# Optimization experiments

Hardware: AMD Instinct MI355X
Metric: run time of the kernel (lower is better)

Reference implementation:

```python
import jax, jax.numpy as jnp
import numpy as np

V, H, W, L, HID = 8, 256, 256, 32, 64
NC, NF = 64, 64
R = 1024


def _grid_sample(img, grid):
    # img [V,C,H,W], grid [V,N,2] with (x,y) in [-1,1]; bilinear, zero padding,
    # align_corners=False (matches torch.nn.functional.grid_sample defaults).
    Vv, C, Hh, Ww = img.shape
    x = (grid[..., 0] + 1.0) * (Ww * 0.5) - 0.5
    y = (grid[..., 1] + 1.0) * (Hh * 0.5) - 0.5
    x0 = jnp.floor(x)
    y0 = jnp.floor(y)
    wx = x - x0
    wy = y - y0
    vidx = jnp.arange(Vv)[:, None]
    def tap(xf, yf):
        valid = (xf >= 0) & (xf <= Ww - 1) & (yf >= 0) & (yf <= Hh - 1)
        xi = jnp.clip(xf, 0, Ww - 1).astype(jnp.int32)
        yi = jnp.clip(yf, 0, Hh - 1).astype(jnp.int32)
        return img[vidx, :, yi, xi] * valid[..., None].astype(img.dtype)  # [V,N,C]
    return (tap(x0, y0) * ((1 - wx) * (1 - wy))[..., None]
            + tap(x0 + 1, y0) * (wx * (1 - wy))[..., None]
            + tap(x0, y0 + 1) * ((1 - wx) * wy)[..., None]
            + tap(x0 + 1, y0 + 1) * (wx * wy)[..., None])  # [V,N,C]


def _sample_pdf(bins, weights, n):
    # NeRF inverse-CDF importance sampling; deterministic midpoint u's.
    w = weights + 1e-5                              # [R, M]
    pdf = w / w.sum(-1, keepdims=True)
    cdf = jnp.concatenate([jnp.zeros_like(pdf[:, :1]), jnp.cumsum(pdf, -1)], -1)  # [R, M+1]
    u = jnp.broadcast_to((jnp.arange(n) + 0.5) / n, (bins.shape[0], n))
    inds = jax.vmap(lambda c, uu: jnp.searchsorted(c, uu, side='right'))(cdf, u)
    below = jnp.clip(inds - 1, 0, cdf.shape[-1] - 1)
    above = jnp.clip(inds, 0, cdf.shape[-1] - 1)
    cdf0 = jnp.take_along_axis(cdf, below, -1)
    cdf1 = jnp.take_along_axis(cdf, above, -1)
    bin0 = jnp.take_along_axis(bins, below, -1)
    bin1 = jnp.take_along_axis(bins, above, -1)
    denom = jnp.where(cdf1 - cdf0 < 1e-5, 1.0, cdf1 - cdf0)
    t = (u - cdf0) / denom
    return bin0 + t * (bin1 - bin0)


def _ibrnet(raw_rgb, feat, src_dirc, ray_dirc, W1, b1, W2, b2, Wd, bd, Wb, bb):
    # IBRNet-style per-view MLP + cross-view pooling for density, softmax
    # blending of source colors for rgb.
    x = jnp.concatenate([raw_rgb, feat, src_dirc,
                         jnp.broadcast_to(ray_dirc[:, None, :], src_dirc.shape)], -1)  # [P,V,3+L+3+3]
    h = jax.nn.relu(x @ W1 + b1)
    h = jax.nn.relu(h @ W2 + b2)                    # [P,V,HID]
    pooled = jnp.concatenate([h.mean(1), h.var(1)], -1)  # [P,2*HID]
    density = pooled @ Wd + bd                      # [P,1]
    blend = jax.nn.softmax((h @ Wb + bb)[..., 0], axis=1)  # [P,V]
    rgb = jnp.einsum('pv,pvc->pc', blend, raw_rgb)  # [P,3]
    return density, rgb


def _composite(depth, density, rgb):
    # NeRF alpha compositing along samples.
    delta = jnp.concatenate([depth[:, 1:] - depth[:, :-1],
                             jnp.full_like(depth[:, :1], 1e10)], -1)
    alpha = 1.0 - jnp.exp(-jax.nn.relu(density) * delta)
    trans = jnp.cumprod(1.0 - alpha + 1e-10, -1)
    trans = jnp.concatenate([jnp.ones_like(trans[:, :1]), trans[:, :-1]], -1)
    w = alpha * trans                               # [R,S]
    return w, (w[..., None] * rgb).sum(1), (w * depth).sum(1), w.sum(1)


def setup_inputs():
    rng = np.random.default_rng(0)

    def look_at(pos):
        pos = np.asarray(pos, np.float64)
        z = -pos / np.linalg.norm(pos)
        up = np.array([0.0, 0.0, 1.0])
        x = np.cross(up, z); x /= np.linalg.norm(x)
        y = np.cross(z, x)
        Rm = np.stack([x, y, z], 0)
        return np.concatenate([Rm, (-Rm @ pos)[:, None]], 1).astype(np.float32)

    ang = np.linspace(0, 2 * np.pi, V, endpoint=False)
    cam_pos = np.stack([3 * np.cos(ang), 3 * np.sin(ang), 0.3 * np.ones(V)], 1)
    E = np.stack([look_at(p) for p in cam_pos], 0)              # [V,3,4]
    f = 300.0
    K = np.broadcast_to(np.array([[f, 0, W / 2], [0, f, H / 2], [0, 0, 1]], np.float32), (V, 3, 3)).copy()

    o = np.array([3.2, 0.1, 0.2], np.float32)
    targets = rng.uniform(-0.2, 0.2, (R, 3)).astype(np.float32)  # points near head center
    d = targets - o
    d /= np.linalg.norm(d, axis=1, keepdims=True)
    dist = float(np.linalg.norm(o))
    near = np.full((R, 1), dist - 0.5, np.float32)
    far = np.full((R, 1), dist + 0.5, np.float32)
    ray = np.concatenate([np.broadcast_to(o, (R, 3)), d, near, far], 1).astype(np.float32)

    inp = {
        'ray': jnp.asarray(ray),
        'source_intrinsic': jnp.asarray(K),
        'source_extrinsic': jnp.asarray(E),
        'source_cam_pos': jnp.asarray(cam_pos.astype(np.float32)),
        'source_shape': jnp.full((V, 2), float(H), jnp.float32),
        'source_mask': jnp.ones((V, 1, H, W), jnp.float32),
        'source_image': jnp.asarray(rng.random((V, 3, H, W), dtype=np.float32)),
        'source_feature': jnp.asarray(rng.standard_normal((V, 2 * L, H, W), dtype=np.float32) * 0.1),
    }
    in_dim = 3 + L + 3 + 3

    def mlp(prefix):
        return {
            prefix + 'W1': jnp.asarray(rng.standard_normal((in_dim, HID), dtype=np.float32) * 0.1),
            prefix + 'b1': jnp.asarray(rng.standard_normal(HID, dtype=np.float32) * 0.01),
            prefix + 'W2': jnp.asarray(rng.standard_normal((HID, HID), dtype=np.float32) * 0.1),
            prefix + 'b2': jnp.asarray(rng.standard_normal(HID, dtype=np.float32) * 0.01),
            prefix + 'Wd': jnp.asarray(rng.standard_normal((2 * HID, 1), dtype=np.float32) * 0.1),
            prefix + 'bd': jnp.asarray(rng.standard_normal(1, dtype=np.float32) * 0.01),
            prefix + 'Wb': jnp.asarray(rng.standard_normal((HID, 1), dtype=np.float32) * 0.1),
            prefix + 'bb': jnp.asarray(rng.standard_normal(1, dtype=np.float32) * 0.01),
        }
    inp.update(mlp('c'))
    inp.update(mlp('f'))
    return inp


def reference(ray, source_intrinsic, source_extrinsic, source_cam_pos, source_shape,
              source_mask, source_image, source_feature,
              cW1, cb1, cW2, cb2, cWd, cbd, cWb, cbb,
              fW1, fb1, fW2, fb2, fWd, fbd, fWb, fbb):
    o, d = ray[:, :3], ray[:, 3:6]
    near, far = ray[:, 6:7], ray[:, 7:8]
    P = jnp.einsum('vij,vjk->vik', source_intrinsic, source_extrinsic)  # [V,3,4]
    wh = source_shape[:, ::-1]                                          # (W,H) per view

    def sample_point(depth):                    # depth [R,S]
        pos = o[:, None, :] + d[:, None, :] * depth[..., None]          # [R,S,3]
        dn = d / jnp.linalg.norm(d, axis=-1, keepdims=True)
        dirc = jnp.broadcast_to(dn[:, None, :], pos.shape)
        pos_h = jnp.concatenate([pos, jnp.ones_like(pos[..., :1])], -1)
        pix = jnp.einsum('rsk,vck->rsvc', pos_h, P)                     # [R,S,V,3]
        pix = pix[..., :2] / (pix[..., 2:3] + 1e-6)
        pix = 2.0 * (pix / wh[None, None]) - 1.0
        return pos, -dirc, pix

    def compute_color(pos, dirc, pix, W1, b1, W2, b2, Wd, bd, Wb, bb, fs, fe):
        Rr, Ss = pix.shape[0], pix.shape[1]
        grid = pix.reshape(Rr * Ss, -1, 2).transpose(1, 0, 2)           # [V,P,2]
        m = _grid_sample(source_mask, grid)[..., 0]                     # [V,P]
        hull = m.sum(0) > (source_mask.shape[0] - 1e-3)                 # visual hull: inside all views
        raw_rgb = _grid_sample(source_image, grid).transpose(1, 0, 2)   # [P,V,3]
        feat = _grid_sample(source_feature, grid)[..., fs:fe].transpose(1, 0, 2)  # [P,V,L]
        pos_f = pos.reshape(-1, 3)
        sd = source_cam_pos[None] - pos_f[:, None]
        sd = sd / jnp.linalg.norm(sd, axis=-1, keepdims=True)
        dens, rgb = _ibrnet(raw_rgb, feat, sd, dirc.reshape(-1, 3), W1, b1, W2, b2, Wd, bd, Wb, bb)
        dens = jnp.where(hull, dens[:, 0], 0.0).reshape(Rr, Ss)
        rgb = jnp.where(hull[:, None], rgb, 0.0).reshape(Rr, Ss, 3)
        return dens, rgb

    # coarse stratified sampling (deterministic bin midpoints)
    t = (jnp.arange(NC) + 0.5) / NC
    c_depth = near + (far - near) * t[None]                             # [R,NC]
    c_pos, c_dir, c_pix = sample_point(c_depth)
    c_dens, c_rgbp = compute_color(c_pos, c_dir, c_pix, cW1, cb1, cW2, cb2, cWd, cbd, cWb, cbb, 0, L)
    c_w, c_rgb, c_dep, c_alp = _composite(c_depth, c_dens, c_rgbp)

    # fine importance sampling from coarse weights
    mids = 0.5 * (c_depth[:, 1:] + c_depth[:, :-1])
    f_depth = _sample_pdf(mids, jax.lax.stop_gradient(c_w[:, 1:-1]), NF)
    full_depth = jnp.sort(jnp.concatenate([c_depth, f_depth], -1), -1)  # [R,NC+NF]
    f_pos, f_dir, f_pix = sample_point(full_depth)
    f_dens, f_rgbp = compute_color(f_pos, f_dir, f_pix, fW1, fb1, fW2, fb2, fWd, fbd, fWb, fbb, L, 2 * L)
    _, f_rgb, f_dep, f_alp = _composite(full_depth, f_dens, f_rgbp)
    return c_rgb, c_dep, c_alp, f_rgb, f_dep, f_alp
```

## Files before the change

### kernel.cpp

```cpp
#include <hip/hip_runtime.h>
#include <hip/hip_bf16.h>
#include <math.h>

#define V_   8
#define H_   256
#define W_   256
#define L_   32
#define HID_ 64
#define NC_  64
#define NF_  64
#define R_   1024
#define IND_ 41
#define HW_  (H_*W_)

typedef __attribute__((ext_vector_type(8)))  short short8v;
typedef __attribute__((ext_vector_type(16))) float f32x16;

__device__ __forceinline__ unsigned int pk2bf(float a, float b) {
    unsigned int ra = (unsigned int)__bfloat16_as_ushort(__float2bfloat16(a));
    unsigned int rb = (unsigned int)__bfloat16_as_ushort(__float2bfloat16(b));
    return ra | (rb << 16);
}

template<int CTRL>
__device__ __forceinline__ float dpp_add(float x) {
    int m = __builtin_amdgcn_mov_dpp(__builtin_bit_cast(int, x), CTRL, 0xF, 0xF, true);
    return x + __builtin_bit_cast(float, m);
}
template<int CTRL>
__device__ __forceinline__ float dpp_max(float x) {
    int m = __builtin_amdgcn_mov_dpp(__builtin_bit_cast(int, x), CTRL, 0xF, 0xF, true);
    return fmaxf(x, __builtin_bit_cast(float, m));
}
__device__ __forceinline__ float swz_xor4(float x) {
    int m = __builtin_amdgcn_ds_swizzle(__builtin_bit_cast(int, x), 0x101F);
    return __builtin_bit_cast(float, m);
}
__device__ __forceinline__ float vsum8(float x) {
    x = dpp_add<0xB1>(x);
    x = dpp_add<0x4E>(x);
    x += swz_xor4(x);
    return x;
}
__device__ __forceinline__ float vmax8(float x) {
    x = dpp_max<0xB1>(x);
    x = dpp_max<0x4E>(x);
    x = fmaxf(x, swz_xor4(x));
    return x;
}
__device__ __forceinline__ float redsum64(float x) {
    #pragma unroll
    for (int off = 32; off >= 1; off >>= 1) x += __shfl_xor(x, off, 64);
    return x;
}
__device__ __forceinline__ float scan_mul64(float x, int lane) {
    #pragma unroll
    for (int off = 1; off < 64; off <<= 1) {
        float y = __shfl_up(x, off, 64);
        x = (lane >= off) ? x * y : x;
    }
    return x;
}
__device__ __forceinline__ float scan_add64(float x, int lane) {
    #pragma unroll
    for (int off = 1; off < 64; off <<= 1) {
        float y = __shfl_up(x, off, 64);
        x = (lane >= off) ? x + y : x;
    }
    return x;
}

__device__ __forceinline__ void packMFMA_body(
    int t, const float* __restrict__ W1, const float* __restrict__ b1,
    const float* __restrict__ W2, const float* __restrict__ b2,
    const float* __restrict__ Wd, const float* __restrict__ Wb,
    unsigned int* __restrict__ out) {
    if (t < 1536) {
        int blk = t >> 8, idx = t & 255;
        int mt = blk / 3, kt = blk % 3;
        int l = idx >> 2, rg = idx & 3;
        int hi = l >> 5;
        int j  = 32 * mt + (l & 31);
        int k0 = 16 * kt + 8 * hi + 2 * rg;
        int k1 = k0 + 1;
        float v0 = (k0 < 41) ? W1[k0 * 64 + j] : (k0 == 41 ? b1[j] : 0.f);
        float v1 = (k1 < 41) ? W1[k1 * 64 + j] : (k1 == 41 ? b1[j] : 0.f);
        out[t] = pk2bf(v0, v1);
    } else if (t < 3584) {
        int u = t - 1536;
        int blk = u >> 8, idx = u & 255;
        int l = idx >> 2, rg = idx & 3;
        int hi = l >> 5;
        int j2 = 32 * (blk >> 2) + (l & 31);
        int k0 = 16 * (blk & 3) + 8 * hi + 2 * rg;
        out[t] = pk2bf(W2[k0 * 64 + j2], W2[(k0 + 1) * 64 + j2]);
    } else if (t < 3840) {
        int i = t - 3584;
        int w = i >> 6, mt = (i >> 5) & 1, hi = (i >> 4) & 1, rg = i & 15;
        int j2 = (rg & 3) + 8 * (rg >> 2) + 4 * hi + 32 * mt;
        float v = (w == 0) ? b2[j2] : (w == 1) ? Wb[j2] : (w == 2) ? Wd[j2] : Wd[64 + j2];
        ((float*)out)[t] = v;
    }
}

__global__ __launch_bounds__(256) void k_init(
    const float* __restrict__ Km, const float* __restrict__ Em, float* __restrict__ Pm,
    const float* __restrict__ cW1, const float* __restrict__ cb1,
    const float* __restrict__ cW2, const float* __restrict__ cb2,
    const float* __restrict__ cWd, const float* __restrict__ cWb,
    unsigned int* __restrict__ FRc,
    const float* __restrict__ fW1, const float* __restrict__ fb1,
    const float* __restrict__ fW2, const float* __restrict__ fb2,
    const float* __restrict__ fWd, const float* __restrict__ fWb,
    unsigned int* __restrict__ FRf) {
    const int bid = blockIdx.x, tid = threadIdx.x;
    if (bid == 0) {
        if (tid >= V_ * 12) return;
        int v = tid / 12, e = tid - v * 12, row = e >> 2, col = e & 3;
        float acc = 0.f;
        #pragma unroll
        for (int k = 0; k < 3; ++k)
            acc += Km[v * 9 + row * 3 + k] * Em[v * 12 + k * 4 + col];
        Pm[v * 12 + row * 4 + col] = acc;
    } else if (bid <= 15) {
        packMFMA_body((bid - 1) * 256 + tid, cW1, cb1, cW2, cb2, cWd, cWb, FRc);
    } else if (bid <= 30) {
        packMFMA_body((bid - 16) * 256 + tid, fW1, fb1, fW2, fb2, fWd, fWb, FRf);
    }
}

__global__ __launch_bounds__(256) void k_packB2(const float* __restrict__ msk,
                                                const float* __restrict__ img,
                                                const float* __restrict__ fea,
                                                float* __restrict__ pk) {
    __shared__ unsigned short tile[64][80];
    const int xb = blockIdx.x * 64, y = blockIdx.y, v = blockIdx.z;
    const int t = threadIdx.x;
    const int x = t & 63, cg = t >> 6;
    const size_t px = (size_t)y * W_ + xb + x;
    #pragma unroll
    for (int step = 0; step < 17; ++step) {
        int ch = step * 4 + cg;
        if (ch < 68) {
            float val;
            if (ch == 0)      val = msk[(size_t)v * HW_ + px];
            else if (ch < 4)  val = img[((size_t)(v * 3 + (ch - 1))) * HW_ + px];
            else              val = fea[((size_t)(v * 2 * L_ + (ch - 4))) * HW_ + px];
            unsigned short bf = __bfloat16_as_ushort(__float2bfloat16(val));
            if (ch == 0)      { tile[x][0] = bf; tile[x][40] = bf; }
            else if (ch < 4)  { tile[x][ch] = bf; tile[x][40 + ch] = bf; }
            else if (ch < 36) { tile[x][ch] = bf; }
            else              { tile[x][ch + 8] = bf; }
        }
    }
    if (t < 256) {
        int xi = t >> 2, c = t & 3;
        tile[xi][36 + c] = 0;
        tile[xi][76 + c] = 0;
    }
    __syncthreads();
    uint2* dst = (uint2*)(pk + ((size_t)v * HW_ + (size_t)y * W_ + xb) * 40);
    for (int j = t; j < 1280; j += 256) {
        int p = j / 20, sl = j % 20;
        dst[j] = *(const uint2*)&tile[p][sl * 4];
    }
}

template <int S, bool FINE, int GOFF>
__global__ __launch_bounds__(256) void k_mlp_mfma(
    const float* __restrict__ ray, const float* __restrict__ Pm,
    const float* __restrict__ cam, const float* __restrict__ shp,
    const float* __restrict__ pk,
    const unsigned int* __restrict__ FR,
    const float* __restrict__ bd, const float* __restrict__ bb,
    const float* __restrict__ deptharr,
    float* __restrict__ odens, float* __restrict__ orgb) {

    __shared__ __align__(16) char smem[40960];
    const int lane = threadIdx.x & 63;
    const int wv   = threadIdx.x >> 6;
    const int hi   = lane >> 5;
    const int l31  = lane & 31;
    char* Xw  = smem + wv * 10240;
    char* H1w = Xw + 6144;

    const int pbase = (blockIdx.x * 4 + wv) * 8;
    const int P0 = pbase + (lane >> 3);
    const int v  = lane & 7;
    const int r  = P0 / S, s = P0 - r * S;

    const float ox = ray[r*8+0], oy = ray[r*8+1], oz = ray[r*8+2];
    const float dx = ray[r*8+3], dy = ray[r*8+4], dz = ray[r*8+5];
    const float nv = ray[r*8+6], fv = ray[r*8+7];

    float depth;
    if (FINE) depth = deptharr[P0];
    else      depth = nv + (fv - nv) * ((s + 0.5f) / (float)S);

    const float px = ox + dx*depth, py = oy + dy*depth, pz = oz + dz*depth;
    const float dn = sqrtf(dx*dx + dy*dy + dz*dz);
    const float rdx = -dx/dn, rdy = -dy/dn, rdz = -dz/dn;

    const float* Pv = Pm + v * 12;
    float q0 = Pv[0]*px + Pv[1]*py + Pv[2]*pz  + Pv[3];
    float q1 = Pv[4]*px + Pv[5]*py + Pv[6]*pz  + Pv[7];
    float q2 = Pv[8]*px + Pv[9]*py + Pv[10]*pz + Pv[11];
    float inv = 1.0f / (q2 + 1e-6f);
    float uu = q0 * inv, ww = q1 * inv;
    float gx = 2.0f * (uu / shp[v*2+1]) - 1.0f;
    float gy = 2.0f * (ww / shp[v*2+0]) - 1.0f;
    float sx = (gx + 1.0f) * ((float)W_ * 0.5f) - 0.5f;
    float sy = (gy + 1.0f) * ((float)H_ * 0.5f) - 0.5f;
    float x0f = floorf(sx), y0f = floorf(sy);
    float fx = sx - x0f, fy = sy - y0f;

    int offp[4]; float wt[4];
    {
        float xs[2] = {x0f, x0f + 1.f}, ys[2] = {y0f, y0f + 1.f};
        float wxs[2] = {1.f - fx, fx},  wys[2] = {1.f - fy, fy};
        #pragma unroll
        for (int t = 0; t < 4; ++t) {
            float xf = xs[t & 1], yf = ys[t >> 1];
            bool val = (xf >= 0.f) && (xf <= (float)(W_-1)) &&
                       (yf >= 0.f) && (yf <= (float)(H_-1));
            int xi = (int)fminf(fmaxf(xf, 0.f), (float)(W_-1));
            int yi = (int)fminf(fmaxf(yf, 0.f), (float)(H_-1));
            offp[t] = yi * W_ + xi;
            wt[t] = wxs[t & 1] * wys[t >> 1] * (val ? 1.f : 0.f);
        }
    }

    float vals[40];
    #pragma unroll
    for (int i = 0; i < 40; ++i) vals[i] = 0.f;
    #pragma unroll
    for (int t = 0; t < 4; ++t) {
        const uint4* fp = (const uint4*)pk + ((size_t)v * HW_ + offp[t]) * 10 + GOFF;
        float wtt = wt[t];
        #pragma unroll
        for (int s5 = 0; s5 < 5; ++s5) {
            uint4 q = fp[s5];
            unsigned int dw[4] = {q.x, q.y, q.z, q.w};
            #pragma unroll
            for (int e = 0; e < 4; ++e) {
                int i = s5 * 8 + e * 2;
                vals[i]   += wtt * __uint_as_float(dw[e] << 16);
                vals[i+1] += wtt * __uint_as_float(dw[e] & 0xFFFF0000u);
            }
        }
    }
    float msample = vals[0];
    float rv0 = vals[1], rv1 = vals[2], rv2 = vals[3];
    float sdx = cam[v*3+0]-px, sdy = cam[v*3+1]-py, sdz = cam[v*3+2]-pz;
    float snv = sqrtf(sdx*sdx + sdy*sdy + sdz*sdz);
    sdx /= snv; sdy /= snv; sdz /= snv;

    float xx[42];
    xx[0] = rv0; xx[1] = rv1; xx[2] = rv2;
    #pragma unroll
    for (int k = 0; k < 32; ++k) xx[3+k] = vals[4+k];
    xx[35] = sdx; xx[36] = sdy; xx[37] = sdz;
    xx[38] = rdx; xx[39] = rdy; xx[40] = rdz;
    xx[41] = 1.0f;

    {
        unsigned int d[24];
        #pragma unroll
        for (int i = 0; i < 21; ++i) d[i] = pk2bf(xx[2*i], xx[2*i+1]);
        d[21] = 0u; d[22] = 0u; d[23] = 0u;
        #pragma unroll
        for (int o = 0; o < 6; ++o)
            *(uint4*)(Xw + o * 1024 + lane * 16) =
                make_uint4(d[o*4], d[o*4+1], d[o*4+2], d[o*4+3]);
    }

    short8v aw1[6];
    #pragma unroll
    for (int i = 0; i < 6; ++i)
        aw1[i] = __builtin_bit_cast(short8v, ((const uint4*)FR)[i * 64 + lane]);
    const float4* PL4 = (const float4*)(FR + 3584);
    const float bdv = bd[0], bbv = bb[0];

    float hs = vsum8(msample);
    float hssw  = __shfl_xor(hs, 32, 64);
    float rv0sw = __shfl_xor(rv0, 32, 64);
    float rv1sw = __shfl_xor(rv1, 32, 64);
    float rv2sw = __shfl_xor(rv2, 32, 64);

    #pragma unroll
    for (int nt = 0; nt < 2; ++nt) {
        const int n = nt * 32 + l31;
        f32x16 acc1[2];
        #pragma unroll
        for (int mt = 0; mt < 2; ++mt)
            #pragma unroll
            for (int q = 0; q < 16; ++q) acc1[mt][q] = 0.f;
        #pragma unroll
        for (int kt = 0; kt < 3; ++kt) {
            uint4 bu = *(const uint4*)(Xw + (2*kt + hi) * 1024 + n * 16);
            short8v b = __builtin_bit_cast(short8v, bu);
            acc1[0] = __builtin_amdgcn_mfma_f32_32x32x16_bf16(aw1[kt],     b, acc1[0], 0, 0, 0);
            acc1[1] = __builtin_amdgcn_mfma_f32_32x32x16_bf16(aw1[3 + kt], b, acc1[1], 0, 0, 0);
        }
        #pragma unroll
        for (int mt = 0; mt < 2; ++mt)
            #pragma unroll
            for (int q = 0; q < 4; ++q) {
                unsigned int w0 = pk2bf(fmaxf(acc1[mt][4*q+0], 0.f),
                                        fmaxf(acc1[mt][4*q+1], 0.f));
                unsigned int w1 = pk2bf(fmaxf(acc1[mt][4*q+2], 0.f),
                                        fmaxf(acc1[mt][4*q+3], 0.f));
                *(uint2*)(H1w + (q + 4*mt) * 512 + l31 * 16 + hi * 8) = make_uint2(w0, w1);
            }
        short8v aw2[8];
        #pragma unroll
        for (int i = 0; i < 8; ++i)
            aw2[i] = __builtin_bit_cast(short8v, ((const uint4*)(FR + 1536))[i * 64 + lane]);
        f32x16 acc2[2];
        #pragma unroll
        for (int mt = 0; mt < 2; ++mt)
            #pragma unroll
            for (int q4 = 0; q4 < 4; ++q4) {
                float4 c = PL4[(mt*2 + hi)*4 + q4];
                acc2[mt][4*q4+0] = c.x; acc2[mt][4*q4+1] = c.y;
                acc2[mt][4*q4+2] = c.z; acc2[mt][4*q4+3] = c.w;
            }
        #pragma unroll
        for (int kt = 0; kt < 4; ++kt) {
            uint4 bu = *(const uint4*)(H1w + (2*kt + hi) * 512 + l31 * 16);
            short8v b = __builtin_bit_cast(short8v, bu);
            acc2[0] = __builtin_amdgcn_mfma_f32_32x32x16_bf16(aw2[kt],     b, acc2[0], 0, 0, 0);
            acc2[1] = __builtin_amdgcn_mfma_f32_32x32x16_bf16(aw2[4 + kt], b, acc2[1], 0, 0, 0);
        }

        float lgp = 0.f, dacc = 0.f, cacc = 0.f;
        #pragma unroll
        for (int mt = 0; mt < 2; ++mt)
            #pragma unroll
            for (int q4 = 0; q4 < 4; ++q4) {
                float4 wb4 = PL4[16 + (mt*2 + hi)*4 + q4];
                float4 wd4 = PL4[32 + (mt*2 + hi)*4 + q4];
                float4 w24 = PL4[48 + (mt*2 + hi)*4 + q4];
                #pragma unroll
                for (int e = 0; e < 4; ++e) {
                    float hv = fmaxf(acc2[mt][4*q4+e], 0.f);
                    float wbv = (e==0)?wb4.x:(e==1)?wb4.y:(e==2)?wb4.z:wb4.w;
                    float wdv = (e==0)?wd4.x:(e==1)?wd4.y:(e==2)?wd4.z:wd4.w;
                    float w2v = (e==0)?w24.x:(e==1)?w24.y:(e==2)?w24.z:w24.w;
                    lgp  += hv * wbv;
                    dacc += hv * wdv + hv * hv * w2v;
                    float sj = vsum8(hv);
                    cacc += sj * sj * w2v;
                }
            }
        float lg = lgp + __shfl_xor(lgp, 32, 64) + bbv;
        dacc += __shfl_xor(dacc, 32, 64);
        dacc  = vsum8(dacc);
        cacc += __shfl_xor(cacc, 32, 64);
        float density = dacc * 0.125f - cacc * (1.0f / 64.0f) + bdv;

        float mx = vmax8(lg);
        float e  = expf(lg - mx);
        float es = vsum8(e);
        float r0c = (hi == nt) ? rv0 : rv0sw;
        float r1c = (hi == nt) ? rv1 : rv1sw;
        float r2c = (hi == nt) ? rv2 : rv2sw;
        float br  = vsum8(e * r0c);
        float bg  = vsum8(e * r1c);
        float bbl = vsum8(e * r2c);
        float hn  = (nt == 0) ? hs : hssw;
        bool hull = hn > ((float)V_ - 0.001f);

        if ((lane & 0x27) == 0) {
            int PP = pbase + 4 * nt + (lane >> 3);
            float is = 1.0f / es;
            odens[PP]      = hull ? density  : 0.f;
            orgb[PP*3 + 0] = hull ? br  * is : 0.f;
            orgb[PP*3 + 1] = hull ? bg  * is : 0.f;
            orgb[PP*3 + 2] = hull ? bbl * is : 0.f;
        }
    }
}

template <int S, int FS, bool FINE>
__global__ __launch_bounds__(256, 2) void k_mlp_fb(
    const float* __restrict__ ray, const float* __restrict__ Pm,
    const float* __restrict__ cam, const float* __restrict__ shp,
    const float* __restrict__ msk, const float* __restrict__ img,
    const float* __restrict__ fea,
    const float* __restrict__ W1, const float* __restrict__ b1,
    const float* __restrict__ W2, const float* __restrict__ b2,
    const float* __restrict__ Wd, const float* __restrict__ bd,
    const float* __restrict__ Wb, const float* __restrict__ bb,
    const float* __restrict__ deptharr,
    float* __restrict__ odens, float* __restrict__ orgb) {

    const int tid = blockIdx.x * 256 + threadIdx.x;
    const int v   = tid & 7;
    const int P   = tid >> 3;
    const int r   = P / S, s = P - r * S;

    const float ox = ray[r*8+0], oy = ray[r*8+1], oz = ray[r*8+2];
    const float dx = ray[r*8+3], dy = ray[r*8+4], dz = ray[r*8+5];
    const float nv = ray[r*8+6], fv = ray[r*8+7];
    float depth;
    if (FINE) depth = deptharr[P];
    else      depth = nv + (fv - nv) * ((s + 0.5f) / (float)S);
    const float px = ox + dx*depth, py = oy + dy*depth, pz = oz + dz*depth;
    const float dn = sqrtf(dx*dx + dy*dy + dz*dz);
    const float rdx = -dx/dn, rdy = -dy/dn, rdz = -dz/dn;
    const float* Pv = Pm + v * 12;
    float q0 = Pv[0]*px + Pv[1]*py + Pv[2]*pz  + Pv[3];
    float q1 = Pv[4]*px + Pv[5]*py + Pv[6]*pz  + Pv[7];
    float q2 = Pv[8]*px + Pv[9]*py + Pv[10]*pz + Pv[11];
    float inv = 1.0f / (q2 + 1e-6f);
    float uu = q0 * inv, ww = q1 * inv;
    float gx = 2.0f * (uu / shp[v*2+1]) - 1.0f;
    float gy = 2.0f * (ww / shp[v*2+0]) - 1.0f;
    float sx = (gx + 1.0f) * ((float)W_ * 0.5f) - 0.5f;
    float sy = (gy + 1.0f) * ((float)H_ * 0.5f) - 0.5f;
    float x0f = floorf(sx), y0f = floorf(sy);
    float fx = sx - x0f, fy = sy - y0f;
    int offp[4]; float wt[4];
    {
        float xs[2] = {x0f, x0f + 1.f}, ys[2] = {y0f, y0f + 1.f};
        float wxs[2] = {1.f - fx, fx},  wys[2] = {1.f - fy, fy};
        #pragma unroll
        for (int t = 0; t < 4; ++t) {
            float xf = xs[t & 1], yf = ys[t >> 1];
            bool val = (xf >= 0.f) && (xf <= (float)(W_-1)) &&
                       (yf >= 0.f) && (yf <= (float)(H_-1));
            int xi = (int)fminf(fmaxf(xf, 0.f), (float)(W_-1));
            int yi = (int)fminf(fmaxf(yf, 0.f), (float)(H_-1));
            offp[t] = yi * W_ + xi;
            wt[t] = wxs[t & 1] * wys[t >> 1] * (val ? 1.f : 0.f);
        }
    }
    const float* mb = msk + v * HW_;
    float msample = wt[0]*mb[offp[0]] + wt[1]*mb[offp[1]]
                  + wt[2]*mb[offp[2]] + wt[3]*mb[offp[3]];
    float rv0 = 0.f, rv1 = 0.f, rv2 = 0.f;
    {
        const float* ib = img + (v * 3) * HW_;
        #pragma unroll
        for (int t = 0; t < 4; ++t) {
            rv0 += wt[t] * ib[offp[t]];
            rv1 += wt[t] * ib[HW_ + offp[t]];
            rv2 += wt[t] * ib[2 * HW_ + offp[t]];
        }
    }
    float sdx = cam[v*3+0]-px, sdy = cam[v*3+1]-py, sdz = cam[v*3+2]-pz;
    float snv = sqrtf(sdx*sdx + sdy*sdy + sdz*sdz);
    sdx /= snv; sdy /= snv; sdz /= snv;
    float xx[IND_];
    xx[0] = rv0; xx[1] = rv1; xx[2] = rv2;
    #pragma unroll
    for (int k = 0; k < 32; ++k) {
        const float* fb = fea + (size_t)(v * (2*L_) + FS + k) * HW_;
        xx[3+k] = wt[0]*fb[offp[0]] + wt[1]*fb[offp[1]]
                + wt[2]*fb[offp[2]] + wt[3]*fb[offp[3]];
    }
    xx[35] = sdx; xx[36] = sdy; xx[37] = sdz;
    xx[38] = rdx; xx[39] = rdy; xx[40] = rdz;
    float h1[HID_];
    #pragma unroll
    for (int j = 0; j < HID_; ++j) {
        float a0 = 0.f;
        #pragma unroll
        for (int k = 0; k < IND_; ++k) a0 += xx[k] * W1[k * HID_ + j];
        h1[j] = fmaxf(b1[j] + a0, 0.f);
    }
    float lg = bb[0];
    float A = 0.f, B = 0.f, C = 0.f;
    #pragma unroll 1
    for (int j = 0; j < HID_; j += 4) {
        float hh[4];
        #pragma unroll
        for (int jj = 0; jj < 4; ++jj) {
            float a0 = 0.f;
            #pragma unroll
            for (int k = 0; k < HID_; ++k) a0 += h1[k] * W2[k * HID_ + (j + jj)];
            hh[jj] = fmaxf(b2[j + jj] + a0, 0.f);
        }
        #pragma unroll
        for (int jj = 0; jj < 4; ++jj) {
            float h = hh[jj];
            lg += h * Wb[j + jj];
            A  += h * Wd[j + jj];
            B  += h * h * Wd[HID_ + j + jj];
            float sj = vsum8(h);
            C  += sj * sj * Wd[HID_ + j + jj];
        }
    }
    A = vsum8(A); B = vsum8(B);
    float density = A * 0.125f + B * 0.125f - C * (1.0f / 64.0f) + bd[0];
    float hsv = vsum8(msample);
    bool hull = hsv > ((float)V_ - 0.001f);
    float mx = vmax8(lg);
    float e = expf(lg - mx);
    float es = vsum8(e);
    float br  = vsum8(e * rv0);
    float bg  = vsum8(e * rv1);
    float bbl = vsum8(e * rv2);
    if (v == 0) {
        float is = 1.0f / es;
        odens[P]      = hull ? density  : 0.f;
        orgb[P*3 + 0] = hull ? br  * is : 0.f;
        orgb[P*3 + 1] = hull ? bg  * is : 0.f;
        orgb[P*3 + 2] = hull ? bbl * is : 0.f;
    }
}

__global__ __launch_bounds__(256) void k_comp_coarse(const float* __restrict__ ray,
                                                     const float* __restrict__ dens,
                                                     const float* __restrict__ rgb,
                                                     float* __restrict__ out,
                                                     float* __restrict__ fulld) {
    __shared__ float cdfS[4][64];
    __shared__ float fdS[4][64];
    const int wv = threadIdx.x >> 6, lane = threadIdx.x & 63;
    const int r = blockIdx.x * 4 + wv;
    const float nv = ray[r*8+6], fv = ray[r*8+7];
    const int s = lane;

    float d0 = nv + (fv - nv) * ((s + 0.5f) / NC_);
    float d1 = nv + (fv - nv) * ((s + 1.5f) / NC_);
    float delta = (s == NC_-1) ? 1e10f : (d1 - d0);
    float a = 1.f - expf(-fmaxf(dens[r*NC_ + s], 0.f) * delta);
    float qv = 1.f - a + 1e-10f;
    float inc = scan_mul64(qv, lane);
    float trans = __shfl_up(inc, 1, 64);
    if (lane == 0) trans = 1.f;
    float w = a * trans;

    float g0 = rgb[(r*NC_+s)*3+0], g1 = rgb[(r*NC_+s)*3+1], g2 = rgb[(r*NC_+s)*3+2];
    float c0 = redsum64(w * g0);
    float c1 = redsum64(w * g1);
    float c2 = redsum64(w * g2);
    float cd = redsum64(w * d0);
    float ca = redsum64(w);
    if (lane == 0) {
        out[r*3+0] = c0; out[r*3+1] = c1; out[r*3+2] = c2;
        out[3072 + r] = cd;
        out[4096 + r] = ca;
    }

    float pw = (s >= 1 && s <= 62) ? (w + 1e-5f) : 0.f;
    float tot = redsum64(pw);
    float p = pw / tot;
    float ic = scan_add64(p, lane);
    cdfS[wv][lane] = ic;
    __syncthreads();

    float u = (lane + 0.5f) / NF_;
    int lo = 0, hi = 63;
    while (lo < hi) {
        int mid = (lo + hi) >> 1;
        if (cdfS[wv][mid] <= u) lo = mid + 1; else hi = mid;
    }
    int below = lo - 1;
    int above = (lo > 62) ? 62 : lo;
    float cA = cdfS[wv][below], cB = cdfS[wv][above];
    float b0 = nv + (fv - nv) * ((below + 1.0f) / NC_);
    float b1 = nv + (fv - nv) * ((above + 1.0f) / NC_);
    float dnm = cB - cA;
    dnm = (dnm < 1e-5f) ? 1.f : dnm;
    float fdv = b0 + (u - cA) / dnm * (b1 - b0);
    fdS[wv][lane] = fdv;
    __syncthreads();

    lo = 0; hi = 64;
    while (lo < hi) {
        int mid = (lo + hi) >> 1;
        if (fdS[wv][mid] < d0) lo = mid + 1; else hi = mid;
    }
    fulld[r*128 + s + lo] = d0;

    lo = 0; hi = 64;
    while (lo < hi) {
        int mid = (lo + hi) >> 1;
        float daj = nv + (fv - nv) * ((mid + 0.5f) / NC_);
        if (daj <= fdv) lo = mid + 1; else hi = mid;
    }
    fulld[r*128 + lane + lo] = fdv;
}

__global__ __launch_bounds__(256) void k_comp_fine(const float* __restrict__ fulld,
                                                   const float* __restrict__ dens,
                                                   const float* __restrict__ rgb,
                                                   float* __restrict__ out) {
    const int wv = threadIdx.x >> 6, lane = threadIdx.x & 63;
    const int r = blockIdx.x * 4 + wv;
    const int S = NC_ + NF_;
    const float* fl = fulld + r * S;
    const int s0 = 2 * lane, s1 = 2 * lane + 1;

    float f0 = fl[s0], f1 = fl[s1];
    float nx = __shfl_down(f0, 1, 64);
    float dl0 = f1 - f0;
    float dl1 = (lane == 63) ? 1e10f : (nx - f1);
    float a0 = 1.f - expf(-fmaxf(dens[r*S + s0], 0.f) * dl0);
    float a1 = 1.f - expf(-fmaxf(dens[r*S + s1], 0.f) * dl1);
    float q0 = 1.f - a0 + 1e-10f, q1 = 1.f - a1 + 1e-10f;
    float inc = scan_mul64(q0 * q1, lane);
    float E = __shfl_up(inc, 1, 64);
    if (lane == 0) E = 1.f;
    float w0 = a0 * E, w1 = a1 * (E * q0);

    float g00 = rgb[(r*S+s0)*3+0], g01 = rgb[(r*S+s0)*3+1], g02 = rgb[(r*S+s0)*3+2];
    float g10 = rgb[(r*S+s1)*3+0], g11 = rgb[(r*S+s1)*3+1], g12 = rgb[(r*S+s1)*3+2];
    float c0 = redsum64(w0*g00 + w1*g10);
    float c1 = redsum64(w0*g01 + w1*g11);
    float c2 = redsum64(w0*g02 + w1*g12);
    float cd = redsum64(w0*f0 + w1*f1);
    float ca = redsum64(w0 + w1);
    if (lane == 0) {
        out[5120 + r*3+0] = c0; out[5120 + r*3+1] = c1; out[5120 + r*3+2] = c2;
        out[8192 + r] = cd;
        out[9216 + r] = ca;
    }
}

extern "C" void kernel_launch(void* const* d_in, const int* in_sizes, int n_in,
                              void* d_out, int out_size, void* d_ws, size_t ws_size,
                              hipStream_t stream) {
    const float* ray = (const float*)d_in[0];
    const float* Kin = (const float*)d_in[1];
    const float* Ein = (const float*)d_in[2];
    const float* cam = (const float*)d_in[3];
    const float* shp = (const float*)d_in[4];
    const float* msk = (const float*)d_in[5];
    const float* img = (const float*)d_in[6];
    const float* fea = (const float*)d_in[7];
    const float* cw[8]; for (int i = 0; i < 8; ++i) cw[i] = (const float*)d_in[8+i];
    const float* fw[8]; for (int i = 0; i < 8; ++i) fw[i] = (const float*)d_in[16+i];

    float* ws    = (float*)d_ws;
    float* Pm    = ws;
    unsigned int* FRc = (unsigned int*)(Pm + 96);
    unsigned int* FRf = FRc + 4096;
    float* cdens = (float*)(FRf + 4096);
    float* crgb  = cdens + R_ * NC_;
    float* fulld = crgb + R_ * NC_ * 3;
    float* fdens = fulld + R_ * (NC_+NF_);
    float* frgb  = fdens + R_ * (NC_+NF_);
    float* pk    = frgb + R_ * (NC_+NF_) * 3;

    size_t base_floats = (size_t)(pk - ws);
    size_t need = (base_floats + (size_t)V_ * HW_ * 40 + 64) * sizeof(float);
    bool packed = (ws_size >= need);

    float* outp  = (float*)d_out;

    if (packed) {
        k_init<<<31, 256, 0, stream>>>(Kin, Ein, Pm,
            cw[0], cw[1], cw[2], cw[3], cw[4], cw[6], FRc,
            fw[0], fw[1], fw[2], fw[3], fw[4], fw[6], FRf);
        k_packB2<<<dim3(W_/64, H_, V_), 256, 0, stream>>>(msk, img, fea, pk);

        k_mlp_mfma<NC_, false, 0><<<R_ * NC_ / 32, 256, 0, stream>>>(
            ray, Pm, cam, shp, pk, FRc, cw[5], cw[7],
            nullptr, cdens, crgb);

        k_comp_coarse<<<R_ / 4, 256, 0, stream>>>(ray, cdens, crgb, outp, fulld);

        k_mlp_mfma<NC_ + NF_, true, 5><<<R_ * (NC_+NF_) / 32, 256, 0, stream>>>(
            ray, Pm, cam, shp, pk, FRf, fw[5], fw[7],
            fulld, fdens, frgb);

        k_comp_fine<<<R_ / 4, 256, 0, stream>>>(fulld, fdens, frgb, outp);
    } else {
        k_init<<<1, 256, 0, stream>>>(Kin, Ein, Pm,
            cw[0], cw[1], cw[2], cw[3], cw[4], cw[6], FRc,
            fw[0], fw[1], fw[2], fw[3], fw[4], fw[6], FRf);
        k_mlp_fb<NC_, 0, false><<<R_ * NC_ * 8 / 256, 256, 0, stream>>>(
            ray, Pm, cam, shp, msk, img, fea,
            cw[0], cw[1], cw[2], cw[3], cw[4], cw[5], cw[6], cw[7],
            nullptr, cdens, crgb);

        k_comp_coarse<<<R_ / 4, 256, 0, stream>>>(ray, cdens, crgb, outp, fulld);

        k_mlp_fb<NC_ + NF_, L_, true><<<R_ * (NC_+NF_) * 8 / 256, 256, 0, stream>>>(
            ray, Pm, cam, shp, msk, img, fea,
            fw[0], fw[1], fw[2], fw[3], fw[4], fw[5], fw[6], fw[7],
            fulld, fdens, frgb);

        k_comp_fine<<<R_ / 4, 256, 0, stream>>>(fulld, fdens, frgb, outp);
    }
}
```

Measured before the change: 193.0 us.

## Switch packed features and MLP MFMAs from bf16 to fp16 with packed bilinear accumulation

Converts the packed feature texture, the weight fragments and the hidden activations from bf16 to fp16, and switches the MFMA instructions to the f16 variant. Bilinear interpolation now accumulates directly in packed half2 vectors, so the results feed the MFMA input without unpack and repack steps. The W1 layout shifts by one row so the packed vector positions line up with the mask slot. This removes per-element conversion and float accumulation work in the gather loop, at the cost of accumulating in fp16, which can lose precision or overflow on large feature values.

Result: faster. 186.5 us (-3.3%).

```diff
diff --git a/kernel.cpp b/kernel.cpp
--- a/kernel.cpp
+++ b/kernel.cpp
@@ -13,13 +13,13 @@
 #define IND_ 41
 #define HW_  (H_*W_)
 
-typedef __attribute__((ext_vector_type(8)))  short short8v;
+typedef _Float16 h2v __attribute__((ext_vector_type(2)));
+typedef _Float16 h8v __attribute__((ext_vector_type(8)));
 typedef __attribute__((ext_vector_type(16))) float f32x16;
 
-__device__ __forceinline__ unsigned int pk2bf(float a, float b) {
-    unsigned int ra = (unsigned int)__bfloat16_as_ushort(__float2bfloat16(a));
-    unsigned int rb = (unsigned int)__bfloat16_as_ushort(__float2bfloat16(b));
-    return ra | (rb << 16);
+__device__ __forceinline__ unsigned int pk2hf(float a, float b) {
+    h2v t; t[0] = (_Float16)a; t[1] = (_Float16)b;
+    return __builtin_bit_cast(unsigned int, t);
 }
 
 template<int CTRL>
@@ -83,9 +83,13 @@
         int j  = 32 * mt + (l & 31);
         int k0 = 16 * kt + 8 * hi + 2 * rg;
         int k1 = k0 + 1;
-        float v0 = (k0 < 41) ? W1[k0 * 64 + j] : (k0 == 41 ? b1[j] : 0.f);
-        float v1 = (k1 < 41) ? W1[k1 * 64 + j] : (k1 == 41 ? b1[j] : 0.f);
-        out[t] = pk2bf(v0, v1);
+        auto w1v = [&](int k) -> float {
+            if (k == 0) return 0.f;
+            if (k <= 41) return W1[(k - 1) * 64 + j];
+            if (k == 42) return b1[j];
+            return 0.f;
+        };
+        out[t] = pk2hf(w1v(k0), w1v(k1));
     } else if (t < 3584) {
         int u = t - 1536;
         int blk = u >> 8, idx = u & 255;
@@ -93,7 +97,7 @@
         int hi = l >> 5;
         int j2 = 32 * (blk >> 2) + (l & 31);
         int k0 = 16 * (blk & 3) + 8 * hi + 2 * rg;
-        out[t] = pk2bf(W2[k0 * 64 + j2], W2[(k0 + 1) * 64 + j2]);
+        out[t] = pk2hf(W2[k0 * 64 + j2], W2[(k0 + 1) * 64 + j2]);
     } else if (t < 3840) {
         int i = t - 3584;
         int w = i >> 6, mt = (i >> 5) & 1, hi = (i >> 4) & 1, rg = i & 15;
@@ -146,7 +150,7 @@
             if (ch == 0)      val = msk[(size_t)v * HW_ + px];
             else if (ch < 4)  val = img[((size_t)(v * 3 + (ch - 1))) * HW_ + px];
             else              val = fea[((size_t)(v * 2 * L_ + (ch - 4))) * HW_ + px];
-            unsigned short bf = __bfloat16_as_ushort(__float2bfloat16(val));
+            unsigned short bf = __builtin_bit_cast(unsigned short, (_Float16)val);
             if (ch == 0)      { tile[x][0] = bf; tile[x][40] = bf; }
             else if (ch < 4)  { tile[x][ch] = bf; tile[x][40 + ch] = bf; }
             else if (ch < 36) { tile[x][ch] = bf; }
@@ -230,54 +234,55 @@
         }
     }
 
-    float vals[40];
-    #pragma unroll
-    for (int i = 0; i < 40; ++i) vals[i] = 0.f;
+    h2v vals[18];
+    #pragma unroll
+    for (int i = 0; i < 18; ++i) vals[i] = (h2v){(_Float16)0.f, (_Float16)0.f};
+    float msample = 0.f;
     #pragma unroll
     for (int t = 0; t < 4; ++t) {
         const uint4* fp = (const uint4*)pk + ((size_t)v * HW_ + offp[t]) * 10 + GOFF;
-        float wtt = wt[t];
+        float wf = wt[t];
+        _Float16 wh = (_Float16)wf;
+        h2v w2 = (h2v){wh, wh};
         #pragma unroll
         for (int s5 = 0; s5 < 5; ++s5) {
             uint4 q = fp[s5];
             unsigned int dw[4] = {q.x, q.y, q.z, q.w};
+            if (s5 == 0) {
+                h2v m2 = __builtin_bit_cast(h2v, dw[0]);
+                msample += wf * (float)m2[0];
+            }
             #pragma unroll
             for (int e = 0; e < 4; ++e) {
-                int i = s5 * 8 + e * 2;
-                vals[i]   += wtt * __uint_as_float(dw[e] << 16);
-                vals[i+1] += wtt * __uint_as_float(dw[e] & 0xFFFF0000u);
+                int i = s5 * 4 + e;
+                if (i < 18) vals[i] += w2 * __builtin_bit_cast(h2v, dw[e]);
             }
         }
     }
-    float msample = vals[0];
-    float rv0 = vals[1], rv1 = vals[2], rv2 = vals[3];
+    float rv0 = (float)vals[0][1], rv1 = (float)vals[1][0], rv2 = (float)vals[1][1];
     float sdx = cam[v*3+0]-px, sdy = cam[v*3+1]-py, sdz = cam[v*3+2]-pz;
     float snv = sqrtf(sdx*sdx + sdy*sdy + sdz*sdz);
     sdx /= snv; sdy /= snv; sdz /= snv;
 
-    float xx[42];
-    xx[0] = rv0; xx[1] = rv1; xx[2] = rv2;
-    #pragma unroll
-    for (int k = 0; k < 32; ++k) xx[3+k] = vals[4+k];
-    xx[35] = sdx; xx[36] = sdy; xx[37] = sdz;
-    xx[38] = rdx; xx[39] = rdy; xx[40] = rdz;
-    xx[41] = 1.0f;
-
     {
         unsigned int d[24];
         #pragma unroll
-        for (int i = 0; i < 21; ++i) d[i] = pk2bf(xx[2*i], xx[2*i+1]);
-        d[21] = 0u; d[22] = 0u; d[23] = 0u;
+        for (int i = 0; i < 18; ++i) d[i] = __builtin_bit_cast(unsigned int, vals[i]);
+        d[18] = pk2hf(sdx, sdy);
+        d[19] = pk2hf(sdz, rdx);
+        d[20] = pk2hf(rdy, rdz);
+        d[21] = pk2hf(1.0f, 0.f);
+        d[22] = 0u; d[23] = 0u;
         #pragma unroll
         for (int o = 0; o < 6; ++o)
             *(uint4*)(Xw + o * 1024 + lane * 16) =
                 make_uint4(d[o*4], d[o*4+1], d[o*4+2], d[o*4+3]);
     }
 
-    short8v aw1[6];
+    h8v aw1[6];
     #pragma unroll
     for (int i = 0; i < 6; ++i)
-        aw1[i] = __builtin_bit_cast(short8v, ((const uint4*)FR)[i * 64 + lane]);
+        aw1[i] = __builtin_bit_cast(h8v, ((const uint4*)FR)[i * 64 + lane]);
     const float4* PL4 = (const float4*)(FR + 3584);
     const float bdv = bd[0], bbv = bb[0];
 
@@ -298,24 +303,24 @@
         #pragma unroll
         for (int kt = 0; kt < 3; ++kt) {
             uint4 bu = *(const uint4*)(Xw + (2*kt + hi) * 1024 + n * 16);
-            short8v b = __builtin_bit_cast(short8v, bu);
-            acc1[0] = __builtin_amdgcn_mfma_f32_32x32x16_bf16(aw1[kt],     b, acc1[0], 0, 0, 0);
-            acc1[1] = __builtin_amdgcn_mfma_f32_32x32x16_bf16(aw1[3 + kt], b, acc1[1], 0, 0, 0);
+            h8v b = __builtin_bit_cast(h8v, bu);
+            acc1[0] = __builtin_amdgcn_mfma_f32_32x32x16_f16(aw1[kt],     b, acc1[0], 0, 0, 0);
+            acc1[1] = __builtin_amdgcn_mfma_f32_32x32x16_f16(aw1[3 + kt], b, acc1[1], 0, 0, 0);
         }
         #pragma unroll
         for (int mt = 0; mt < 2; ++mt)
             #pragma unroll
             for (int q = 0; q < 4; ++q) {
-                unsigned int w0 = pk2bf(fmaxf(acc1[mt][4*q+0], 0.f),
+                unsigned int w0 = pk2hf(fmaxf(acc1[mt][4*q+0], 0.f),
                                         fmaxf(acc1[mt][4*q+1], 0.f));
-                unsigned int w1 = pk2bf(fmaxf(acc1[mt][4*q+2], 0.f),
+                unsigned int w1 = pk2hf(fmaxf(acc1[mt][4*q+2], 0.f),
                                         fmaxf(acc1[mt][4*q+3], 0.f));
                 *(uint2*)(H1w + (q + 4*mt) * 512 + l31 * 16 + hi * 8) = make_uint2(w0, w1);
             }
-        short8v aw2[8];
+        h8v aw2[8];
         #pragma unroll
         for (int i = 0; i < 8; ++i)
-            aw2[i] = __builtin_bit_cast(short8v, ((const uint4*)(FR + 1536))[i * 64 + lane]);
+            aw2[i] = __builtin_bit_cast(h8v, ((const uint4*)(FR + 1536))[i * 64 + lane]);
         f32x16 acc2[2];
         #pragma unroll
         for (int mt = 0; mt < 2; ++mt)
@@ -328,9 +333,9 @@
         #pragma unroll
         for (int kt = 0; kt < 4; ++kt) {
             uint4 bu = *(const uint4*)(H1w + (2*kt + hi) * 512 + l31 * 16);
-            short8v b = __builtin_bit_cast(short8v, bu);
-            acc2[0] = __builtin_amdgcn_mfma_f32_32x32x16_bf16(aw2[kt],     b, acc2[0], 0, 0, 0);
-            acc2[1] = __builtin_amdgcn_mfma_f32_32x32x16_bf16(aw2[4 + kt], b, acc2[1], 0, 0, 0);
+            h8v b = __builtin_bit_cast(h8v, bu);
+            acc2[0] = __builtin_amdgcn_mfma_f32_32x32x16_f16(aw2[kt],     b, acc2[0], 0, 0, 0);
+            acc2[1] = __builtin_amdgcn_mfma_f32_32x32x16_f16(aw2[4 + kt], b, acc2[1], 0, 0, 0);
         }
 
         float lgp = 0.f, dacc = 0.f, cacc = 0.f;
```
